# Optimization experiments

Measured on AMD Instinct MI355X. Metric: run time of the kernel, lower is better.

## Reference

```python
import jax, jax.numpy as jnp
import numpy as np

N_NODES = 100000
N_EDGES = 1600000
IN_FEATS = 128
HIDDEN = 128
OUT_DIM = 128


def setup_inputs() -> dict:
    key = jax.random.key(0)
    ks = jax.random.split(key, 8)
    x = jax.random.normal(ks[0], (N_NODES, IN_FEATS), dtype=jnp.float32)
    W1 = jax.random.normal(ks[1], (IN_FEATS, HIDDEN), dtype=jnp.float32) * (1.0 / np.sqrt(IN_FEATS))
    b1 = jnp.zeros((HIDDEN,), dtype=jnp.float32)
    W2 = jax.random.normal(ks[2], (HIDDEN, HIDDEN), dtype=jnp.float32) * (1.0 / np.sqrt(HIDDEN))
    b2 = jnp.zeros((HIDDEN,), dtype=jnp.float32)
    W3 = jax.random.normal(ks[3], (HIDDEN, OUT_DIM), dtype=jnp.float32) * (1.0 / np.sqrt(HIDDEN))
    b3 = jnp.zeros((OUT_DIM,), dtype=jnp.float32)
    edge_src = jax.random.randint(ks[4], (N_EDGES,), 0, N_NODES, dtype=jnp.int32)
    edge_dst = jax.random.randint(ks[5], (N_EDGES,), 0, N_NODES, dtype=jnp.int32)
    return {"x": x, "W1": W1, "b1": b1, "W2": W2, "b2": b2, "W3": W3, "b3": b3,
            "edge_src": edge_src, "edge_dst": edge_dst}


def _mean_agg(h, edge_src, edge_dst, inv_deg):
    # gather src features, scatter-sum to dst, divide by in-degree (mean)
    summed = jax.ops.segment_sum(h[edge_src], edge_dst, num_segments=N_NODES)
    return summed * inv_deg[:, None]


def reference(x, W1, b1, W2, b2, W3, b3, edge_src, edge_dst):
    # in-degree (clamped to 1 to avoid div-by-zero, matching mean over empty = 0)
    deg = jax.ops.segment_sum(jnp.ones((N_EDGES,), dtype=jnp.float32), edge_dst,
                              num_segments=N_NODES)
    inv_deg = 1.0 / jnp.maximum(deg, 1.0)

    # DGL GINConv (eps=0, mean): h = Linear(h + mean_neighbors(h))
    h = x
    h = (h + _mean_agg(h, edge_src, edge_dst, inv_deg)) @ W1 + b1
    h = jax.nn.relu(h)  # dropout inactive in eval mode
    h = (h + _mean_agg(h, edge_src, edge_dst, inv_deg)) @ W2 + b2
    h = jax.nn.relu(h)
    h = (h + _mean_agg(h, edge_src, edge_dst, inv_deg)) @ W3 + b3
    return h
```

## Files before the change

kernel.cpp:

```cpp
#include <hip/hip_runtime.h>
#include <hip/hip_bf16.h>
#include <stdint.h>

#if __has_builtin(__builtin_amdgcn_cvt_pk_f32_fp8) && __has_builtin(__builtin_amdgcn_cvt_pk_fp8_f32)
#define FP8_HW 1
#else
#define FP8_HW 0
#include <hip/hip_fp8.h>
#endif

#define N_NODES 100000
#define N_EDGES 1600000
#define FEAT 128

#define BKT_SHIFT 8
#define BKT_SIZE  256
#define NB_BKT    391
#define BKT_CAP   5664
#define NB_SC     800
#define EPB_SC    2000

#define PREP_CVT 6250
#define PREP_W   192
#define PREP_H   800

typedef uint16_t u16;
typedef uint32_t u32;
typedef __attribute__((ext_vector_type(8))) short bf16x8;
typedef __attribute__((ext_vector_type(4))) float f32x4;
typedef __attribute__((ext_vector_type(2))) float f32x2;

__device__ __forceinline__ u16 bf16_rn(float f){
  u32 u = __float_as_uint(f);
  u += 0x7FFFu + ((u >> 16) & 1u);
  return (u16)(u >> 16);
}
__device__ __forceinline__ float bf16_lo(u32 p){ return __uint_as_float(p << 16); }
__device__ __forceinline__ float bf16_hi(u32 p){ return __uint_as_float(p & 0xFFFF0000u); }

__device__ __forceinline__ void fp8x4_to_f32(u32 w, float* o){
#if FP8_HW
  f32x2 a = __builtin_amdgcn_cvt_pk_f32_fp8(w, false);
  f32x2 b = __builtin_amdgcn_cvt_pk_f32_fp8(w, true);
  o[0] = a.x; o[1] = a.y; o[2] = b.x; o[3] = b.y;
#else
  #pragma unroll
  for (int i = 0; i < 4; ++i){
    __hip_fp8_e4m3 t; t.__x = (uint8_t)((w >> (8 * i)) & 0xFF);
    o[i] = (float)t;
  }
#endif
}
__device__ __forceinline__ u32 f32x4_to_fp8(float a, float b, float c, float d){
#if FP8_HW
  u32 r = __builtin_amdgcn_cvt_pk_fp8_f32(a, b, 0, false);
  r = __builtin_amdgcn_cvt_pk_fp8_f32(c, d, r, true);
  return r;
#else
  __hip_fp8_e4m3 qa(a), qb(b), qc(c), qd(d);
  return (u32)qa.__x | ((u32)qb.__x << 8) | ((u32)qc.__x << 16) | ((u32)qd.__x << 24);
#endif
}

__device__ __forceinline__ void acc_row(uint2 r, f32x2* acc){
#if FP8_HW
  acc[0] += __builtin_amdgcn_cvt_pk_f32_fp8(r.x, false);
  acc[1] += __builtin_amdgcn_cvt_pk_f32_fp8(r.x, true);
  acc[2] += __builtin_amdgcn_cvt_pk_f32_fp8(r.y, false);
  acc[3] += __builtin_amdgcn_cvt_pk_f32_fp8(r.y, true);
#else
  float t0[4], t1[4];
  fp8x4_to_f32(r.x, t0); fp8x4_to_f32(r.y, t1);
  acc[0].x += t0[0]; acc[0].y += t0[1]; acc[1].x += t0[2]; acc[1].y += t0[3];
  acc[2].x += t1[0]; acc[2].y += t1[1]; acc[3].x += t1[2]; acc[3].y += t1[3];
#endif
}


__global__ __launch_bounds__(256) void prep_kernel(
    const float* __restrict__ x,
    const float* __restrict__ W1, const float* __restrict__ W2,
    const float* __restrict__ W3, const int* __restrict__ edst,
    uint2* __restrict__ X8, u16* __restrict__ Wp1, u16* __restrict__ Wp2,
    u16* __restrict__ Wp3, int* __restrict__ hcnt, int* __restrict__ ghist){
  __shared__ int h[NB_BKT];
  int blk = blockIdx.x;
  if (blk < PREP_CVT){
    int i = blk * 256 + threadIdx.x;
    const float4* p = (const float4*)x + (size_t)i * 2;
    float4 a = p[0], b = p[1];
    uint2 o;
    o.x = f32x4_to_fp8(a.x, a.y, a.z, a.w);
    o.y = f32x4_to_fp8(b.x, b.y, b.z, b.w);
    X8[i] = o;
  } else if (blk < PREP_CVT + PREP_W){
    int b = blk - PREP_CVT;
    int which = b >> 6;
    const float* W = (which == 0) ? W1 : (which == 1) ? W2 : W3;
    u16*        Wp = (which == 0) ? Wp1 : (which == 1) ? Wp2 : Wp3;
    int idx = (b & 63) * 256 + threadIdx.x;
    int j    = idx & 7;
    int lane = (idx >> 3) & 63;
    int t    = idx >> 9;
    int k0 = t & 3, n0 = t >> 2;
    int k = k0 * 32 + (lane >> 4) * 8 + j;
    int n = n0 * 16 + (lane & 15);
    Wp[idx] = bf16_rn(W[k * FEAT + n]);
  } else if (blk < PREP_CVT + PREP_W + PREP_H){
    int hb = blk - (PREP_CVT + PREP_W);
    for (int i = threadIdx.x; i < NB_BKT; i += 256) h[i] = 0;
    __syncthreads();
    int base = hb * EPB_SC;
    for (int e = base + threadIdx.x; e < base + EPB_SC; e += 256)
      atomicAdd(&h[edst[e] >> BKT_SHIFT], 1);
    __syncthreads();
    for (int i = threadIdx.x; i < NB_BKT; i += 256)
      hcnt[hb * NB_BKT + i] = h[i];
  } else {
    if (threadIdx.x < 64) ghist[threadIdx.x] = 0;
  }
}


__global__ void hscan_kernel(int* __restrict__ hcnt, int* __restrict__ cursor){
  __shared__ int s[256];
  int b = blockIdx.x, t = threadIdx.x;
  int v[4]; int sum = 0;
  #pragma unroll
  for (int j = 0; j < 4; ++j){
    int blk = 4 * t + j;
    v[j] = (blk < NB_SC) ? hcnt[blk * NB_BKT + b] : 0;
    sum += v[j];
  }
  s[t] = sum;
  __syncthreads();
  for (int d = 1; d < 256; d <<= 1){
    int add = (t >= d) ? s[t - d] : 0;
    __syncthreads();
    s[t] += add;
    __syncthreads();
  }
  int excl = s[t] - sum;
  #pragma unroll
  for (int j = 0; j < 4; ++j){
    int blk = 4 * t + j;
    if (blk < NB_SC){ hcnt[blk * NB_BKT + b] = excl; excl += v[j]; }
  }
  if (t == 255) cursor[b] = s[255];
}

__global__ __launch_bounds__(512) void scatter_kernel(const int* __restrict__ src,
                                                      const int* __restrict__ dst,
                                                      const int* __restrict__ hcnt,
                                                      u32* __restrict__ bbuf){
  __shared__ int cur[NB_BKT];
  for (int i = threadIdx.x; i < NB_BKT; i += 512)
    cur[i] = hcnt[blockIdx.x * NB_BKT + i];
  __syncthreads();
  int base = blockIdx.x * EPB_SC;
  for (int e = base + threadIdx.x; e < base + EPB_SC; e += 512){
    int d = dst[e];
    int b = d >> BKT_SHIFT;
    int p = atomicAdd(&cur[b], 1);
    bbuf[(size_t)b * BKT_CAP + p] = (u32)src[e] | ((u32)(d & (BKT_SIZE - 1)) << 24);
  }
}

__global__ __launch_bounds__(1024) void csr_build_kernel(const u32* __restrict__ bbuf,
                                 const int* __restrict__ cursor,
                                 int* __restrict__ offs, int* __restrict__ deg,
                                 float* __restrict__ inv_deg, int* __restrict__ eidx){
  __shared__ u32 bloc[BKT_CAP];
  __shared__ int hist[BKT_SIZE];
  __shared__ int s[BKT_SIZE];
  __shared__ int cu[BKT_SIZE];
  __shared__ int stot;
  int b = blockIdx.x;
  int t = threadIdx.x;
  int lo = b * BKT_CAP;
  int n  = cursor[b];
  for (int e = t; e < n; e += 1024) bloc[e] = bbuf[lo + e];
  if (t < BKT_SIZE) hist[t] = 0;
  __syncthreads();
  for (int e = t; e < n; e += 1024)
    atomicAdd(&hist[bloc[e] >> 24], 1);
  __syncthreads();
  int v = 0, pv = 0;
  if (t < BKT_SIZE){
    v  = hist[t];
    pv = (v + 7) & ~7;
    s[t] = pv;
  }
  __syncthreads();
  for (int d = 1; d < BKT_SIZE; d <<= 1){
    int add = (t < BKT_SIZE && t >= d) ? s[t - d] : 0;
    __syncthreads();
    if (t < BKT_SIZE && t >= d) s[t] += add;
    __syncthreads();
  }
  if (t < BKT_SIZE){
    int excl = s[t] - pv;
    int node = b * BKT_SIZE + t;
    if (node < N_NODES){
      offs[node]    = lo + excl;
      deg[node]     = v;
      inv_deg[node] = 1.0f / fmaxf((float)v, 1.0f);
      for (int p = v; p < pv; ++p) eidx[lo + excl + p] = 0;
    }
    s[t]  = excl;
    cu[t] = 0;
    if (t == BKT_SIZE - 1) stot = excl + pv;
  }
  __syncthreads();
  for (int e = t; e < n; e += 1024){
    u32 q = bloc[e];
    int y = (int)(q >> 24);
    int p = atomicAdd(&cu[y], 1);
    eidx[lo + s[y] + p] = (int)(q & 0xFFFFFFu);
  }
  int tot = stot;
  if (t < 32 && tot + 32 <= BKT_CAP) eidx[lo + tot + t] = 0;
}


__global__ __launch_bounds__(256) void dhist_kernel(const int* __restrict__ deg,
                                                    int* __restrict__ ghist){
  __shared__ int lh[64];
  int t = threadIdx.x;
  if (t < 64) lh[t] = 0;
  __syncthreads();
  int i = blockIdx.x * 256 + t;
  if (i < N_NODES)
    atomicAdd(&lh[63 - min(deg[i], 63)], 1);
  __syncthreads();
  if (t < 64 && lh[t]) atomicAdd(&ghist[t], lh[t]);
}

__global__ __launch_bounds__(64) void dscan_kernel(const int* __restrict__ ghist,
                                                   int* __restrict__ gcur){
  __shared__ int s[64];
  int t = threadIdx.x;
  int v = ghist[t];
  s[t] = v;
  __syncthreads();
  for (int d = 1; d < 64; d <<= 1){
    int add = (t >= d) ? s[t - d] : 0;
    __syncthreads();
    s[t] += add;
    __syncthreads();
  }
  gcur[t] = s[t] - v;
}

__global__ __launch_bounds__(256) void dperm_kernel(const int* __restrict__ deg,
                                                    int* __restrict__ gcur,
                                                    int* __restrict__ perm){
  __shared__ int lh[64];
  __shared__ int lb[64];
  int t = threadIdx.x;
  if (t < 64) lh[t] = 0;
  __syncthreads();
  int i = blockIdx.x * 256 + t;
  bool valid = i < N_NODES;
  int k = 0, rank = 0;
  if (valid){
    k = 63 - min(deg[i], 63);
    rank = atomicAdd(&lh[k], 1);
  }
  __syncthreads();
  if (t < 64 && lh[t]) lb[t] = atomicAdd(&gcur[t], lh[t]);
  __syncthreads();
  if (valid) perm[lb[k] + rank] = i;
}


template<int SM, int OUT>
__global__ __launch_bounds__(128, 8) void layer_kernel(
    const u32* __restrict__ n8,
    const u16* __restrict__ hb,
    const float* __restrict__ xf,
    const int* __restrict__ offs,
    const int* __restrict__ deg,
    const float* __restrict__ inv_deg,
    const int* __restrict__ eidx,
    const int* __restrict__ perm,
    const u16* __restrict__ Wp,
    const float* __restrict__ bias,
    u16* __restrict__ Hout,
    u32* __restrict__ H8out,
    float* __restrict__ Fout){
  __shared__ u16 Tt[16 * FEAT];
  __shared__ int nid[16];
  const int tid   = threadIdx.x;
  const int wid   = tid >> 6;
  const int lane  = tid & 63;
  const int nsub  = lane >> 4;
  const int slice = lane & 15;
  const u32* gbase = n8 + slice * 2;

  if (tid < 16) nid[tid] = perm[blockIdx.x * 16 + tid];
  __syncthreads();

  for (int g = 0; g < 2; ++g){
    const int rrow = wid * 8 + (g << 2) + nsub;
    const int node = nid[rrow];
    const int start = offs[node];
    const int cnt   = deg[node];
    const int pcnt  = (cnt + 7) & ~7;
    const int* ep = eidx + start;

    f32x2 acc[4];
    #pragma unroll
    for (int j = 0; j < 4; ++j) acc[j] = (f32x2){0.f, 0.f};

    uint2 rc[8];
    #pragma unroll
    for (int j = 0; j < 8; ++j) rc[j] = make_uint2(0u, 0u);
    if (pcnt > 0){
      uint4 q0 = *(const uint4*)ep;
      uint4 q1 = *(const uint4*)(ep + 4);
      rc[0] = *(const uint2*)(gbase + (size_t)q0.x * 32);
      rc[1] = *(const uint2*)(gbase + (size_t)q0.y * 32);
      rc[2] = *(const uint2*)(gbase + (size_t)q0.z * 32);
      rc[3] = *(const uint2*)(gbase + (size_t)q0.w * 32);
      rc[4] = *(const uint2*)(gbase + (size_t)q1.x * 32);
      rc[5] = *(const uint2*)(gbase + (size_t)q1.y * 32);
      rc[6] = *(const uint2*)(gbase + (size_t)q1.z * 32);
      rc[7] = *(const uint2*)(gbase + (size_t)q1.w * 32);
    }
    uint4 qn1 = *(const uint4*)(ep + 8);
    uint4 qn2 = *(const uint4*)(ep + 12);

    for (int e = 0; e < pcnt; e += 8){
      uint2 rn[8];
      rn[0] = *(const uint2*)(gbase + (size_t)qn1.x * 32);
      rn[1] = *(const uint2*)(gbase + (size_t)qn1.y * 32);
      rn[2] = *(const uint2*)(gbase + (size_t)qn1.z * 32);
      rn[3] = *(const uint2*)(gbase + (size_t)qn1.w * 32);
      rn[4] = *(const uint2*)(gbase + (size_t)qn2.x * 32);
      rn[5] = *(const uint2*)(gbase + (size_t)qn2.y * 32);
      rn[6] = *(const uint2*)(gbase + (size_t)qn2.z * 32);
      rn[7] = *(const uint2*)(gbase + (size_t)qn2.w * 32);
      qn1 = *(const uint4*)(ep + e + 16);
      qn2 = *(const uint4*)(ep + e + 20);
      #pragma unroll
      for (int j = 0; j < 8; ++j) acc_row(rc[j], acc);
      #pragma unroll
      for (int j = 0; j < 8; ++j) rc[j] = rn[j];
    }

    if (pcnt > cnt){
      float f = (float)(pcnt - cnt);
      uint2 rz = *(const uint2*)gbase;
      f32x2 z[4];
      #pragma unroll
      for (int j = 0; j < 4; ++j) z[j] = (f32x2){0.f, 0.f};
      acc_row(rz, z);
      #pragma unroll
      for (int j = 0; j < 4; ++j) acc[j] -= f * z[j];
    }

    const float w = inv_deg[node];
    float self[8];
    if (SM == 1){
      const float* sp = xf + (size_t)node * FEAT + slice * 8;
      float4 a = *(const float4*)sp;
      float4 b = *(const float4*)(sp + 4);
      self[0]=a.x; self[1]=a.y; self[2]=a.z; self[3]=a.w;
      self[4]=b.x; self[5]=b.y; self[6]=b.z; self[7]=b.w;
    } else {
      const u16* sp = hb + (size_t)node * FEAT + slice * 8;
      uint4 s0 = *(const uint4*)sp;
      self[0]=bf16_lo(s0.x); self[1]=bf16_hi(s0.x); self[2]=bf16_lo(s0.y); self[3]=bf16_hi(s0.y);
      self[4]=bf16_lo(s0.z); self[5]=bf16_hi(s0.z); self[6]=bf16_lo(s0.w); self[7]=bf16_hi(s0.w);
    }
    uint4 o;
    o.x = (u32)bf16_rn(self[0] + w*acc[0].x) | ((u32)bf16_rn(self[1] + w*acc[0].y) << 16);
    o.y = (u32)bf16_rn(self[2] + w*acc[1].x) | ((u32)bf16_rn(self[3] + w*acc[1].y) << 16);
    o.z = (u32)bf16_rn(self[4] + w*acc[2].x) | ((u32)bf16_rn(self[5] + w*acc[2].y) << 16);
    o.w = (u32)bf16_rn(self[6] + w*acc[3].x) | ((u32)bf16_rn(self[7] + w*acc[3].y) << 16);
    ((uint4*)Tt)[rrow * 16 + (slice ^ (rrow & 7))] = o;
  }
  __syncthreads();

  const int quad = lane >> 4;
  const int c    = lane & 15;

  bf16x8 A[4];
  #pragma unroll
  for (int k0 = 0; k0 < 4; ++k0){
    uint4 t = ((const uint4*)Tt)[c * 16 + ((quad + k0 * 4) ^ (c & 7))];
    A[k0] = *(const bf16x8*)&t;
  }
  if (OUT == 0) __syncthreads();

  f32x4 acc2[4];
  #pragma unroll
  for (int i = 0; i < 4; ++i) acc2[i] = (f32x4){0.f, 0.f, 0.f, 0.f};
  #pragma unroll
  for (int i = 0; i < 4; ++i){
    int n0 = wid * 4 + i;
    #pragma unroll
    for (int k0 = 0; k0 < 4; ++k0){
      bf16x8 b = *(const bf16x8*)(Wp + (size_t)(((n0 << 2) | k0) * 64 + lane) * 8);
      acc2[i] = __builtin_amdgcn_mfma_f32_16x16x32_bf16(A[k0], b, acc2[i], 0, 0, 0);
    }
  }
  #pragma unroll
  for (int i = 0; i < 4; ++i){
    int n0 = wid * 4 + i;
    float bv = bias[n0 * 16 + c];
    #pragma unroll
    for (int r = 0; r < 4; ++r){
      int rr  = quad * 4 + r;
      int col = n0 * 16 + c;
      if (OUT == 1){
        Fout[(size_t)nid[rr] * FEAT + col] = acc2[i][r] + bv;
      } else {
        float v = fmaxf(acc2[i][r] + bv, 0.f);
        Tt[rr * FEAT + (col ^ ((rr & 7) << 3))] = bf16_rn(v);
      }
    }
  }

  if (OUT == 0){
    __syncthreads();
    #pragma unroll
    for (int it = 0; it < 2; ++it){
      int p  = it * 128 + tid;
      int rr = p >> 4, qq = p & 15;
      int node = nid[rr];
      uint4 d = ((const uint4*)Tt)[rr * 16 + (qq ^ (rr & 7))];
      *(uint4*)(Hout + (size_t)node * FEAT + qq * 8) = d;
      uint2 o8;
      o8.x = f32x4_to_fp8(bf16_lo(d.x), bf16_hi(d.x), bf16_lo(d.y), bf16_hi(d.y));
      o8.y = f32x4_to_fp8(bf16_lo(d.z), bf16_hi(d.z), bf16_lo(d.w), bf16_hi(d.w));
      *(uint2*)(H8out + (size_t)node * 32 + qq * 2) = o8;
    }
  }
}


static inline size_t align_up(size_t x){ return (x + 255) & ~(size_t)255; }

extern "C" void kernel_launch(void* const* d_in, const int* in_sizes, int n_in,
                              void* d_out, int out_size, void* d_ws, size_t ws_size,
                              hipStream_t stream){
  const float* x  = (const float*)d_in[0];
  const float* W1 = (const float*)d_in[1];
  const float* b1 = (const float*)d_in[2];
  const float* W2 = (const float*)d_in[3];
  const float* b2 = (const float*)d_in[4];
  const float* W3 = (const float*)d_in[5];
  const float* b3 = (const float*)d_in[6];
  const int* esrc = (const int*)d_in[7];
  const int* edst = (const int*)d_in[8];

  char* w = (char*)d_ws;
  int*   deg     = (int*)w;    w += align_up((size_t)N_NODES * 4);
  int*   offs    = (int*)w;    w += align_up((size_t)N_NODES * 4);
  float* inv_deg = (float*)w;  w += align_up((size_t)N_NODES * 4);
  int*   perm    = (int*)w;    w += align_up((size_t)N_NODES * 4);
  int*   ghist   = (int*)w;    w += align_up((size_t)64 * 4);
  int*   gcur    = (int*)w;    w += align_up((size_t)64 * 4);
  int*   eidx    = (int*)w;    w += align_up((size_t)NB_BKT * BKT_CAP * 4);
  u16*   Wp1     = (u16*)w;    w += align_up((size_t)16384 * 2);
  u16*   Wp2     = (u16*)w;    w += align_up((size_t)16384 * 2);
  u16*   Wp3     = (u16*)w;    w += align_up((size_t)16384 * 2);
  u16*   Hb      = (u16*)w;    w += align_up((size_t)N_NODES * FEAT * 2);
  u32*   H8b     = (u32*)w;    w += align_up((size_t)N_NODES * 32 * 4);

  u32* bbuf   = (u32*)Hb;
  int* cursor = (int*)H8b;
  int* hcnt   = (int*)((char*)H8b + align_up((size_t)NB_BKT * 4));

  u16* Ha  = (u16*)d_out;
  u32* H8a = (u32*)((char*)d_out + (size_t)N_NODES * FEAT * 2);
  u32* X8  = (u32*)((char*)d_out + (size_t)N_NODES * FEAT * 3);

  prep_kernel<<<PREP_CVT + PREP_W + PREP_H + 1, 256, 0, stream>>>(
      x, W1, W2, W3, edst, (uint2*)X8, Wp1, Wp2, Wp3, hcnt, ghist);
  hscan_kernel<<<NB_BKT, 256, 0, stream>>>(hcnt, cursor);
  scatter_kernel<<<NB_SC, 512, 0, stream>>>(esrc, edst, hcnt, bbuf);
  csr_build_kernel<<<NB_BKT, 1024, 0, stream>>>(bbuf, cursor, offs, deg, inv_deg, eidx);

  dhist_kernel<<<NB_BKT, 256, 0, stream>>>(deg, ghist);
  dscan_kernel<<<1, 64, 0, stream>>>(ghist, gcur);
  dperm_kernel<<<NB_BKT, 256, 0, stream>>>(deg, gcur, perm);

  const int LAYER_BLOCKS = N_NODES / 16;

  layer_kernel<1, 0><<<LAYER_BLOCKS, 128, 0, stream>>>(
      X8, (const u16*)nullptr, x, offs, deg, inv_deg, eidx, perm, Wp1, b1,
      Ha, H8a, (float*)nullptr);

  layer_kernel<0, 0><<<LAYER_BLOCKS, 128, 0, stream>>>(
      H8a, Ha, (const float*)nullptr, offs, deg, inv_deg, eidx, perm, Wp2, b2,
      Hb, H8b, (float*)nullptr);

  layer_kernel<0, 1><<<LAYER_BLOCKS, 128, 0, stream>>>(
      H8b, Hb, (const float*)nullptr, offs, deg, inv_deg, eidx, perm, Wp3, b3,
      (u16*)nullptr, (u32*)nullptr, (float*)d_out);

  (void)in_sizes; (void)n_in; (void)out_size; (void)ws_size; (void)w;
}
```

Baseline: 323.1 us.

## Drop degree-sorted node permutation and sort neighbor lists by source in CSR build

Removes the three degree-bucketing kernels and the perm indirection so layer blocks process nodes in natural order. The CSR build now stages each bucket's edge list in shared memory and insertion-sorts each node's neighbor list by source id before writing it out. The sorting is meant to improve gather locality and cache reuse, and dropping the permutation saves three launches and an indirect load. In exchange, work per block becomes less balanced across varying degrees, and the serial per-thread insertion sort plus the extra shared array add cost to the CSR build and may lower its occupancy.

New measurement: 334.7 us. +3.6%, slower.

```diff
diff --git a/kernel.cpp b/kernel.cpp
--- a/kernel.cpp
+++ b/kernel.cpp
@@ -82,7 +82,7 @@
     const float* __restrict__ W1, const float* __restrict__ W2,
     const float* __restrict__ W3, const int* __restrict__ edst,
     uint2* __restrict__ X8, u16* __restrict__ Wp1, u16* __restrict__ Wp2,
-    u16* __restrict__ Wp3, int* __restrict__ hcnt, int* __restrict__ ghist){
+    u16* __restrict__ Wp3, int* __restrict__ hcnt){
   __shared__ int h[NB_BKT];
   int blk = blockIdx.x;
   if (blk < PREP_CVT){
@@ -106,7 +106,7 @@
     int k = k0 * 32 + (lane >> 4) * 8 + j;
     int n = n0 * 16 + (lane & 15);
     Wp[idx] = bf16_rn(W[k * FEAT + n]);
-  } else if (blk < PREP_CVT + PREP_W + PREP_H){
+  } else {
     int hb = blk - (PREP_CVT + PREP_W);
     for (int i = threadIdx.x; i < NB_BKT; i += 256) h[i] = 0;
     __syncthreads();
@@ -116,8 +116,6 @@
     __syncthreads();
     for (int i = threadIdx.x; i < NB_BKT; i += 256)
       hcnt[hb * NB_BKT + i] = h[i];
-  } else {
-    if (threadIdx.x < 64) ghist[threadIdx.x] = 0;
   }
 }
 
@@ -171,6 +169,7 @@
                                  int* __restrict__ offs, int* __restrict__ deg,
                                  float* __restrict__ inv_deg, int* __restrict__ eidx){
   __shared__ u32 bloc[BKT_CAP];
+  __shared__ int seg[BKT_CAP];
   __shared__ int hist[BKT_SIZE];
   __shared__ int s[BKT_SIZE];
   __shared__ int cu[BKT_SIZE];
@@ -198,14 +197,15 @@
     if (t < BKT_SIZE && t >= d) s[t] += add;
     __syncthreads();
   }
+  int excl = 0, node = -1;
   if (t < BKT_SIZE){
-    int excl = s[t] - pv;
-    int node = b * BKT_SIZE + t;
+    excl = s[t] - pv;
+    node = b * BKT_SIZE + t;
     if (node < N_NODES){
       offs[node]    = lo + excl;
       deg[node]     = v;
       inv_deg[node] = 1.0f / fmaxf((float)v, 1.0f);
-      for (int p = v; p < pv; ++p) eidx[lo + excl + p] = 0;
+      for (int p = v; p < pv; ++p) seg[excl + p] = 0;
     }
     s[t]  = excl;
     cu[t] = 0;
@@ -216,61 +216,24 @@
     u32 q = bloc[e];
     int y = (int)(q >> 24);
     int p = atomicAdd(&cu[y], 1);
-    eidx[lo + s[y] + p] = (int)(q & 0xFFFFFFu);
-  }
+    seg[s[y] + p] = (int)(q & 0xFFFFFFu);
+  }
+  __syncthreads();
+  if (t < BKT_SIZE && node < N_NODES && v > 1){
+    for (int i = 1; i < v; ++i){
+      int key = seg[excl + i];
+      int j = i - 1;
+      while (j >= 0 && seg[excl + j] > key){
+        seg[excl + j + 1] = seg[excl + j];
+        --j;
+      }
+      seg[excl + j + 1] = key;
+    }
+  }
+  __syncthreads();
   int tot = stot;
+  for (int e = t; e < tot; e += 1024) eidx[lo + e] = seg[e];
   if (t < 32 && tot + 32 <= BKT_CAP) eidx[lo + tot + t] = 0;
-}
-
-
-__global__ __launch_bounds__(256) void dhist_kernel(const int* __restrict__ deg,
-                                                    int* __restrict__ ghist){
-  __shared__ int lh[64];
-  int t = threadIdx.x;
-  if (t < 64) lh[t] = 0;
-  __syncthreads();
-  int i = blockIdx.x * 256 + t;
-  if (i < N_NODES)
-    atomicAdd(&lh[63 - min(deg[i], 63)], 1);
-  __syncthreads();
-  if (t < 64 && lh[t]) atomicAdd(&ghist[t], lh[t]);
-}
-
-__global__ __launch_bounds__(64) void dscan_kernel(const int* __restrict__ ghist,
-                                                   int* __restrict__ gcur){
-  __shared__ int s[64];
-  int t = threadIdx.x;
-  int v = ghist[t];
-  s[t] = v;
-  __syncthreads();
-  for (int d = 1; d < 64; d <<= 1){
-    int add = (t >= d) ? s[t - d] : 0;
-    __syncthreads();
-    s[t] += add;
-    __syncthreads();
-  }
-  gcur[t] = s[t] - v;
-}
-
-__global__ __launch_bounds__(256) void dperm_kernel(const int* __restrict__ deg,
-                                                    int* __restrict__ gcur,
-                                                    int* __restrict__ perm){
-  __shared__ int lh[64];
-  __shared__ int lb[64];
-  int t = threadIdx.x;
-  if (t < 64) lh[t] = 0;
-  __syncthreads();
-  int i = blockIdx.x * 256 + t;
-  bool valid = i < N_NODES;
-  int k = 0, rank = 0;
-  if (valid){
-    k = 63 - min(deg[i], 63);
-    rank = atomicAdd(&lh[k], 1);
-  }
-  __syncthreads();
-  if (t < 64 && lh[t]) lb[t] = atomicAdd(&gcur[t], lh[t]);
-  __syncthreads();
-  if (valid) perm[lb[k] + rank] = i;
 }
 
 
@@ -283,27 +246,23 @@
     const int* __restrict__ deg,
     const float* __restrict__ inv_deg,
     const int* __restrict__ eidx,
-    const int* __restrict__ perm,
     const u16* __restrict__ Wp,
     const float* __restrict__ bias,
     u16* __restrict__ Hout,
     u32* __restrict__ H8out,
     float* __restrict__ Fout){
   __shared__ u16 Tt[16 * FEAT];
-  __shared__ int nid[16];
   const int tid   = threadIdx.x;
   const int wid   = tid >> 6;
   const int lane  = tid & 63;
   const int nsub  = lane >> 4;
   const int slice = lane & 15;
+  const int base  = blockIdx.x * 16;
   const u32* gbase = n8 + slice * 2;
-
-  if (tid < 16) nid[tid] = perm[blockIdx.x * 16 + tid];
-  __syncthreads();
 
   for (int g = 0; g < 2; ++g){
     const int rrow = wid * 8 + (g << 2) + nsub;
-    const int node = nid[rrow];
+    const int node = base + rrow;
     const int start = offs[node];
     const int cnt   = deg[node];
     const int pcnt  = (cnt + 7) & ~7;
@@ -415,7 +374,7 @@
       int rr  = quad * 4 + r;
       int col = n0 * 16 + c;
       if (OUT == 1){
-        Fout[(size_t)nid[rr] * FEAT + col] = acc2[i][r] + bv;
+        Fout[(size_t)(base + rr) * FEAT + col] = acc2[i][r] + bv;
       } else {
         float v = fmaxf(acc2[i][r] + bv, 0.f);
         Tt[rr * FEAT + (col ^ ((rr & 7) << 3))] = bf16_rn(v);
@@ -429,7 +388,7 @@
     for (int it = 0; it < 2; ++it){
       int p  = it * 128 + tid;
       int rr = p >> 4, qq = p & 15;
-      int node = nid[rr];
+      int node = base + rr;
       uint4 d = ((const uint4*)Tt)[rr * 16 + (qq ^ (rr & 7))];
       *(uint4*)(Hout + (size_t)node * FEAT + qq * 8) = d;
       uint2 o8;
@@ -460,9 +419,6 @@
   int*   deg     = (int*)w;    w += align_up((size_t)N_NODES * 4);
   int*   offs    = (int*)w;    w += align_up((size_t)N_NODES * 4);
   float* inv_deg = (float*)w;  w += align_up((size_t)N_NODES * 4);
-  int*   perm    = (int*)w;    w += align_up((size_t)N_NODES * 4);
-  int*   ghist   = (int*)w;    w += align_up((size_t)64 * 4);
-  int*   gcur    = (int*)w;    w += align_up((size_t)64 * 4);
   int*   eidx    = (int*)w;    w += align_up((size_t)NB_BKT * BKT_CAP * 4);
   u16*   Wp1     = (u16*)w;    w += align_up((size_t)16384 * 2);
   u16*   Wp2     = (u16*)w;    w += align_up((size_t)16384 * 2);
@@ -478,28 +434,24 @@
   u32* H8a = (u32*)((char*)d_out + (size_t)N_NODES * FEAT * 2);
   u32* X8  = (u32*)((char*)d_out + (size_t)N_NODES * FEAT * 3);
 
-  prep_kernel<<<PREP_CVT + PREP_W + PREP_H + 1, 256, 0, stream>>>(
-      x, W1, W2, W3, edst, (uint2*)X8, Wp1, Wp2, Wp3, hcnt, ghist);
+  prep_kernel<<<PREP_CVT + PREP_W + PREP_H, 256, 0, stream>>>(
+      x, W1, W2, W3, edst, (uint2*)X8, Wp1, Wp2, Wp3, hcnt);
   hscan_kernel<<<NB_BKT, 256, 0, stream>>>(hcnt, cursor);
   scatter_kernel<<<NB_SC, 512, 0, stream>>>(esrc, edst, hcnt, bbuf);
   csr_build_kernel<<<NB_BKT, 1024, 0, stream>>>(bbuf, cursor, offs, deg, inv_deg, eidx);
 
-  dhist_kernel<<<NB_BKT, 256, 0, stream>>>(deg, ghist);
-  dscan_kernel<<<1, 64, 0, stream>>>(ghist, gcur);
-  dperm_kernel<<<NB_BKT, 256, 0, stream>>>(deg, gcur, perm);
-
   const int LAYER_BLOCKS = N_NODES / 16;
 
   layer_kernel<1, 0><<<LAYER_BLOCKS, 128, 0, stream>>>(
-      X8, (const u16*)nullptr, x, offs, deg, inv_deg, eidx, perm, Wp1, b1,
+      X8, (const u16*)nullptr, x, offs, deg, inv_deg, eidx, Wp1, b1,
       Ha, H8a, (float*)nullptr);
 
   layer_kernel<0, 0><<<LAYER_BLOCKS, 128, 0, stream>>>(
-      H8a, Ha, (const float*)nullptr, offs, deg, inv_deg, eidx, perm, Wp2, b2,
+      H8a, Ha, (const float*)nullptr, offs, deg, inv_deg, eidx, Wp2, b2,
       Hb, H8b, (float*)nullptr);
 
   layer_kernel<0, 1><<<LAYER_BLOCKS, 128, 0, stream>>>(
-      H8b, Hb, (const float*)nullptr, offs, deg, inv_deg, eidx, perm, Wp3, b3,
+      H8b, Hb, (const float*)nullptr, offs, deg, inv_deg, eidx, Wp3, b3,
       (u16*)nullptr, (u32*)nullptr, (float*)d_out);
 
   (void)in_sizes; (void)n_in; (void)out_size; (void)ws_size; (void)w;
```
